# Optimization experiments

Measured on AMD Instinct MI355X. Metric: run time of the kernel, lower is better.

## Reference

```python
import jax, jax.numpy as jnp
import numpy as np

N_NEG = 60
TEMP = 0.07

def _normalize(x, axis):
    n = jnp.sqrt(jnp.sum(x * x, axis=axis, keepdims=True))
    return x / jnp.maximum(n, 1e-12)

def _grid_sample(img, grid):
    # img [B,C,H,W], grid [B,h,w,2] in [-1,1]; bilinear, padding_mode='border', align_corners=False
    B, C, H, W = img.shape
    ix = jnp.clip((grid[..., 0] + 1.0) * (W * 0.5) - 0.5, 0.0, W - 1.0)
    iy = jnp.clip((grid[..., 1] + 1.0) * (H * 0.5) - 0.5, 0.0, H - 1.0)
    x0 = jnp.floor(ix); y0 = jnp.floor(iy)
    x1 = jnp.minimum(x0 + 1.0, W - 1.0); y1 = jnp.minimum(y0 + 1.0, H - 1.0)
    wx = (ix - x0)[:, None]; wy = (iy - y0)[:, None]  # [B,1,h,w]
    imgf = img.reshape(B, C, H * W)
    hh, ww = grid.shape[1], grid.shape[2]
    def gat(yy, xx):
        idx = (yy * W + xx).astype(jnp.int32).reshape(B, 1, hh * ww)
        return jnp.take_along_axis(imgf, idx, axis=2).reshape(B, C, hh, ww)
    v00 = gat(y0, x0); v01 = gat(y0, x1); v10 = gat(y1, x0); v11 = gat(y1, x1)
    return (v00 * (1 - wx) * (1 - wy) + v01 * wx * (1 - wy)
            + v10 * (1 - wx) * wy + v11 * wx * wy)

def _forward(ref_fms, tgt_fms, target_l, target_r, queue):
    b, c, h, w = ref_fms.shape
    s = target_l.shape[-1] // w  # integer downscale factor (nearest interpolate == strided slice)
    disps_l = target_l[:, :, ::s, ::s] / float(s)   # [b,1,h,w]
    disps_r = target_r[:, :, ::s, ::s] / float(s)
    xb = jnp.broadcast_to(jnp.linspace(0.0, 1.0, w), (b, h, w))
    yb = jnp.broadcast_to(jnp.linspace(0.0, 1.0, h)[:, None], (b, h, w))

    def warp(img, disp):
        g = jnp.stack([xb + disp[:, 0] / w, yb], axis=-1)
        return _grid_sample(img, 2.0 * g - 1.0)

    # occlusion / validity mask (detached in the original)
    index = jnp.broadcast_to(jnp.arange(w, dtype=ref_fms.dtype), (b, 1, h, w))
    l2r2l = warp(warp(index, disps_r), -disps_l)
    masko = jnp.abs(index - l2r2l)[:, 0] < 3.0
    mask = masko & (disps_l[:, 0] > 0.0) & (xb - disps_l[:, 0] / w >= 0.0)
    mask = jax.lax.stop_gradient(mask).astype(ref_fms.dtype)  # [b,h,w]

    query = _normalize(ref_fms, 1)
    # positive: warp right feature to left view via disparity
    gpos = jnp.stack([xb - disps_l[:, 0] / w, yb], axis=-1)
    positive = _normalize(_grid_sample(tgt_fms, 2.0 * gpos - 1.0), 1)
    l_pos = jnp.einsum('bchw,bchw->bhw', query, positive)[..., None]

    # negatives: random integer pixel shifts around positive location
    # (no n_neg-fold repeat of tgt_fms; vmap grid_sample over the n axis instead)
    k1, k2 = jax.random.split(jax.random.key(1234))
    mag = jax.random.randint(k1, (b, h, w, N_NEG), 1, 25).astype(ref_fms.dtype)
    sgn = jnp.sign(jax.random.uniform(k2, (b, h, w, N_NEG)) - 0.5).astype(ref_fms.dtype)
    x_right = (xb - disps_l[:, 0] / w) * w
    fx = jnp.mod(x_right[..., None] + mag * sgn, float(w)) / w
    fy = fx / h  # faithful to original code (y coord reuses the normalized x coord)
    grids = jnp.moveaxis(jnp.stack([fx, fy], axis=-1), 3, 0)  # [n,b,h,w,2]
    neg = jax.vmap(lambda g: _grid_sample(tgt_fms, 2.0 * g - 1.0))(grids)  # [n,b,c,h,w]
    neg = _normalize(jnp.moveaxis(neg, 0, -1), 1)  # [b,c,h,w,n]
    l_neg = jnp.einsum('bchw,bchwn->bhwn', query, neg)

    qn = _normalize(queue, 0)  # forward re-normalizes the queue each call
    l_q = jnp.einsum('bchw,ck->bhwk', query, jax.lax.stop_gradient(qn))

    logits = jnp.concatenate([l_pos, l_neg, l_q], axis=-1) * mask[..., None]
    logits = logits.reshape(b * h * w, -1) / TEMP
    # CrossEntropyLoss with all-zero labels (positive is class 0)
    return jnp.mean(-jax.nn.log_softmax(logits, axis=-1)[:, 0])

def setup_inputs():
    key = jax.random.key(0)
    k1, k2, k3, k4, k5 = jax.random.split(key, 5)
    b, c, h, w = 2, 128, 64, 128
    H, W = 4 * h, 4 * w
    return {
        'ref_fms': jax.random.normal(k1, (b, c, h, w), jnp.float32),
        'tgt_fms': jax.random.normal(k2, (b, c, h, w), jnp.float32),
        'target_l': jax.random.uniform(k3, (b, 1, H, W), jnp.float32) * 64.0,
        'target_r': jax.random.uniform(k4, (b, 1, H, W), jnp.float32) * 64.0,
        'queue': jax.random.normal(k5, (c, 6000), jnp.float32),
    }

def reference(ref_fms, tgt_fms, target_l, target_r, queue):
    return _forward(ref_fms, tgt_fms, target_l, target_r, queue)
```

## Files before the change

### kernel.cpp

```cpp
#include <hip/hip_runtime.h>
#include <stdint.h>
#include <math.h>

#define HFM 64
#define WFM 128
#define CFM 128
#define BN 2
#define HWFM (HFM*WFM)
#define NPIX (BN*HWFM)
#define KQ 6000
#define KQP 6144
#define NNEG 60
#define NE (NPIX*NNEG)
#define EHALF_U 491520u
#define MSHIFT 15.0f
#define LOG2E 1.4426950408889634f

typedef _Float16 f16_8 __attribute__((ext_vector_type(8)));
typedef _Float16 f16_2 __attribute__((ext_vector_type(2)));
typedef float f32_4 __attribute__((ext_vector_type(4)));

__host__ __device__ __forceinline__ void threefry2x32(uint32_t k0, uint32_t k1,
                                                      uint32_t x0, uint32_t x1,
                                                      uint32_t* o0, uint32_t* o1) {
  uint32_t ks2 = k0 ^ k1 ^ 0x1BD11BDAu;
  x0 += k0; x1 += k1;
#define TFR(r) { x0 += x1; x1 = (x1 << (r)) | (x1 >> (32 - (r))); x1 ^= x0; }
  TFR(13) TFR(15) TFR(26) TFR(6)
  x0 += k1;  x1 += ks2 + 1u;
  TFR(17) TFR(29) TFR(16) TFR(24)
  x0 += ks2; x1 += k0 + 2u;
  TFR(13) TFR(15) TFR(26) TFR(6)
  x0 += k0;  x1 += k1 + 3u;
  TFR(17) TFR(29) TFR(16) TFR(24)
  x0 += k1;  x1 += ks2 + 4u;
  TFR(13) TFR(15) TFR(26) TFR(6)
  x0 += ks2; x1 += k0 + 5u;
#undef TFR
  *o0 = x0; *o1 = x1;
}

__device__ __forceinline__ void gs_coord(float t, float halfdim, float maxc,
                                         int* i0, int* i1, float* w) {
  float g = 2.0f * t - 1.0f;
  float x = (g + 1.0f) * halfdim - 0.5f;
  x = fminf(fmaxf(x, 0.0f), maxc);
  float f = floorf(x);
  *i0 = (int)f;
  *w = x - f;
  *i1 = (int)fminf(f + 1.0f, maxc);
}

__global__ __launch_bounds__(256) void k_A(
    const float* __restrict__ ref, const float* __restrict__ tgt,
    const float* __restrict__ queue,
    const float* __restrict__ target_l, const float* __restrict__ target_r,
    _Float16* __restrict__ refTf, _Float16* __restrict__ tgtTf,
    _Float16* __restrict__ queueTf, float2* __restrict__ qeb,
    float* __restrict__ maskArr, float* __restrict__ xr) {
  __shared__ float tile[64][35];
  int blk = blockIdx.x;
  int tid = threadIdx.x;
  if (blk < 64) {
    int p = blk * 256 + tid;
    int b = p >> 13;
    int rem = p & (HWFM - 1);
    int i = rem >> 7, j = rem & 127;
    const float stepx = 1.0f / 127.0f, stepy = 1.0f / 63.0f;
    float xb = (j == 127) ? 1.0f : j * stepx;
    float yb = (i == 63) ? 1.0f : i * stepy;
    const float* tl = target_l + (size_t)b * 256 * 512;
    const float* tr = target_r + (size_t)b * 256 * 512;
    float dl = tl[(4 * i) * 512 + 4 * j] * 0.25f;
    int y0i, y1i; float wy;
    gs_coord(yb, 32.0f, 63.0f, &y0i, &y1i, &wy);
    float t = xb - dl * (1.0f / 128.0f);
    int x0i, x1i; float wx;
    gs_coord(t, 64.0f, 127.0f, &x0i, &x1i, &wx);
    auto innerv = [&](int y, int x) -> float {
      float xbx = (x == 127) ? 1.0f : x * stepx;
      float drv = tr[(4 * y) * 512 + 4 * x] * 0.25f;
      float ti = xbx + drv * (1.0f / 128.0f);
      float g = 2.0f * ti - 1.0f;
      float ix2 = fminf(fmaxf((g + 1.0f) * 64.0f - 0.5f, 0.0f), 127.0f);
      float x0f = floorf(ix2);
      float wxp = ix2 - x0f;
      float x1f = fminf(x0f + 1.0f, 127.0f);
      return x0f * (1.0f - wxp) + x1f * wxp;
    };
    float v00 = innerv(y0i, x0i), v01 = innerv(y0i, x1i);
    float v10 = innerv(y1i, x0i), v11 = innerv(y1i, x1i);
    float l2r2l = v00 * (1.0f - wx) * (1.0f - wy) + v01 * wx * (1.0f - wy)
                + v10 * (1.0f - wx) * wy + v11 * wx * wy;
    bool masko = fabsf((float)j - l2r2l) < 3.0f;
    bool mk = masko && (dl > 0.0f) && (t >= 0.0f);
    maskArr[p] = mk ? 1.0f : 0.0f;
    xr[p] = t * 128.0f;
  } else if (blk < 88) {
    int k = (blk - 64) * 256 + tid;
    if (k < KQP) {
      if (k >= KQ) { qeb[k] = make_float2(0.0f, -1000.0f); }
      else {
        float ss = 0.0f;
        for (int c = 0; c < CFM; c++) { float v = queue[c * KQ + k]; ss += v * v; }
        float qi = 1.0f / fmaxf(sqrtf(ss), 1e-12f);
        qeb[k] = make_float2(qi * (LOG2E / 0.07f), -MSHIFT * LOG2E);
      }
    }
  } else if (blk < 472) {
    int q = blk - 88;
    int cy = q / 192, nx = q - cy * 192;
    int n0 = nx * 32, c0 = cy * 64;
    int c = tid >> 2, qq = tid & 3;
    const float* sp = queue + (size_t)(c0 + c) * KQ + n0 + qq * 4;
    if (n0 + 32 <= KQ) {
      float4 v0 = *(const float4*)sp;
      float4 v1 = *(const float4*)(sp + 16);
      tile[c][qq * 4 + 0] = v0.x; tile[c][qq * 4 + 1] = v0.y;
      tile[c][qq * 4 + 2] = v0.z; tile[c][qq * 4 + 3] = v0.w;
      tile[c][qq * 4 + 16] = v1.x; tile[c][qq * 4 + 17] = v1.y;
      tile[c][qq * 4 + 18] = v1.z; tile[c][qq * 4 + 19] = v1.w;
    } else {
#pragma unroll
      for (int k = 0; k < 4; k++) {
        int n = n0 + qq * 4 + k;
        tile[c][qq * 4 + k] = (n < KQ) ? sp[k] : 0.0f;
        tile[c][qq * 4 + 16 + k] = (n + 16 < KQ) ? sp[16 + k] : 0.0f;
      }
    }
    __syncthreads();
    int x = tid >> 3, j8 = tid & 7;
    f16_8 o;
#pragma unroll
    for (int k = 0; k < 8; k++) o[k] = (_Float16)tile[j8 * 8 + k][x];
    *(f16_8*)(queueTf + (size_t)(n0 + x) * CFM + c0 + j8 * 8) = o;
  } else {
    int fblk = blk - 472;
    int z = fblk >> 9, rem2 = fblk & 511;
    int cy = rem2 >> 8, xt = rem2 & 255;
    int x0 = xt * 32, c0 = cy * 64;
    int arr = z >> 1, b = z & 1;
    const float* src = (arr == 0 ? ref : tgt) + (size_t)b * CFM * HWFM;
    _Float16* dst = (arr == 0 ? refTf : tgtTf) + (size_t)b * HWFM * CFM;
    int c = tid >> 2, qq = tid & 3;
    const float* sp = src + (size_t)(c0 + c) * HWFM + x0 + qq * 4;
    float4 v0 = *(const float4*)sp;
    float4 v1 = *(const float4*)(sp + 16);
    tile[c][qq * 4 + 0] = v0.x; tile[c][qq * 4 + 1] = v0.y;
    tile[c][qq * 4 + 2] = v0.z; tile[c][qq * 4 + 3] = v0.w;
    tile[c][qq * 4 + 16] = v1.x; tile[c][qq * 4 + 17] = v1.y;
    tile[c][qq * 4 + 18] = v1.z; tile[c][qq * 4 + 19] = v1.w;
    __syncthreads();
    int x = tid >> 3, j8 = tid & 7;
    f16_8 o;
#pragma unroll
    for (int k = 0; k < 8; k++) o[k] = (_Float16)tile[j8 * 8 + k][x];
    *(f16_8*)(dst + (size_t)(x0 + x) * CFM + c0 + j8 * 8) = o;
  }
}

__global__ __launch_bounds__(256) void k_B(
    const _Float16* __restrict__ refTf, const _Float16* __restrict__ tgtTf,
    _Float16* __restrict__ QTf, float* __restrict__ stats,
    const float* __restrict__ maskArr, const float* __restrict__ xr,
    float* __restrict__ S, float* __restrict__ logit0,
    int* __restrict__ count, int* __restrict__ list) {
  __shared__ int wsum[4];
  int blk = blockIdx.x;
  int tid = threadIdx.x;
  int lane = tid & 63;
  if (blk == 0) {
    int wave = tid >> 6;
    int base_p = tid * 64;
    unsigned long long bits = 0ull;
    const float4* m4 = (const float4*)(maskArr + base_p);
#pragma unroll
    for (int k = 0; k < 16; k++) {
      float4 v = m4[k];
      if (v.x > 0.0f) bits |= 1ull << (4 * k + 0);
      if (v.y > 0.0f) bits |= 1ull << (4 * k + 1);
      if (v.z > 0.0f) bits |= 1ull << (4 * k + 2);
      if (v.w > 0.0f) bits |= 1ull << (4 * k + 3);
    }
    int m = __popcll(bits);
    int scan = m;
#pragma unroll
    for (int off = 1; off < 64; off <<= 1) {
      int n = __shfl_up(scan, off, 64);
      if (lane >= off) scan += n;
    }
    if (lane == 63) wsum[wave] = scan;
    __syncthreads();
    int wbase = 0;
    for (int w = 0; w < wave; w++) wbase += wsum[w];
    int idx = wbase + scan - m;
    for (int k = 0; k < 64; k++) {
      if ((bits >> k) & 1ull) list[idx++] = base_p + k;
    }
    if (tid == 255) *count = idx;
  } else if (blk < 65) {
    int sub = tid >> 6;
    int xg = (blk - 1) * 4 + sub;
    int b = xg >> 7, x = xg & 127;
    int xp = min(x + 1, 127);
    int c2 = lane * 2;
    int base = b * HWFM;
    f16_2 c0  = *(const f16_2*)(tgtTf + (size_t)(base + x) * CFM + c2);
    f16_2 c1  = *(const f16_2*)(tgtTf + (size_t)(base + WFM + x) * CFM + c2);
    f16_2 c0p = *(const f16_2*)(tgtTf + (size_t)(base + xp) * CFM + c2);
    f16_2 c1p = *(const f16_2*)(tgtTf + (size_t)(base + WFM + xp) * CFM + c2);
    float a0 = (float)c0[0], a1 = (float)c0[1];
    float b0 = (float)c1[0], b1 = (float)c1[1];
    float p0 = (float)c0p[0], p1 = (float)c0p[1];
    float q0 = (float)c1p[0], q1 = (float)c1p[1];
    float s[7];
    s[0] = a0 * a0 + a1 * a1;
    s[1] = a0 * b0 + a1 * b1;
    s[2] = b0 * b0 + b1 * b1;
    s[3] = a0 * p0 + a1 * p1;
    s[4] = a0 * q0 + a1 * q1;
    s[5] = b0 * p0 + b1 * p1;
    s[6] = b0 * q0 + b1 * q1;
#pragma unroll
    for (int o = 32; o; o >>= 1)
#pragma unroll
      for (int k = 0; k < 7; k++) s[k] += __shfl_xor(s[k], o, 64);
    if (lane == 0) {
      float* st = stats + (size_t)xg * 8;
#pragma unroll
      for (int k = 0; k < 7; k++) st[k] = s[k];
      st[7] = 0.0f;
    }
  } else {
    int wave = tid >> 6;
    int p = (blk - 65) * 4 + wave;
    float mk = maskArr[p];
    if (mk == 0.0f) return;
    int b = p >> 13;
    int rem = p & (HWFM - 1);
    int i = rem >> 7;
    const float stepy = 1.0f / 63.0f;
    float yb = (i == 63) ? 1.0f : i * stepy;
    float t = xr[p] * (1.0f / 128.0f);
    int y0i, y1i; float wy;
    gs_coord(yb, 32.0f, 63.0f, &y0i, &y1i, &wy);
    int x0i, x1i; float wx;
    gs_coord(t, 64.0f, 127.0f, &x0i, &x1i, &wx);

    int c2 = lane * 2;
    f16_2 q2 = *(const f16_2*)(refTf + (size_t)p * CFM + c2);
    int bo = b * HWFM;
    f16_2 a2 = *(const f16_2*)(tgtTf + (size_t)(bo + y0i * WFM + x0i) * CFM + c2);
    f16_2 b2 = *(const f16_2*)(tgtTf + (size_t)(bo + y0i * WFM + x1i) * CFM + c2);
    f16_2 cc2 = *(const f16_2*)(tgtTf + (size_t)(bo + y1i * WFM + x0i) * CFM + c2);
    f16_2 d2 = *(const f16_2*)(tgtTf + (size_t)(bo + y1i * WFM + x1i) * CFM + c2);

    float w00 = (1.0f - wx) * (1.0f - wy), w01 = wx * (1.0f - wy);
    float w10 = (1.0f - wx) * wy,          w11 = wx * wy;
    float q0 = (float)q2[0], q1 = (float)q2[1];
    float v0 = w00 * (float)a2[0] + w01 * (float)b2[0] + w10 * (float)cc2[0] + w11 * (float)d2[0];
    float v1 = w00 * (float)a2[1] + w01 * (float)b2[1] + w10 * (float)cc2[1] + w11 * (float)d2[1];

    float s0 = q0 * q0 + q1 * q1;
    float s1 = q0 * v0 + q1 * v1;
    float s2 = v0 * v0 + v1 * v1;
#pragma unroll
    for (int o = 32; o; o >>= 1) {
      s0 += __shfl_xor(s0, o, 64);
      s1 += __shfl_xor(s1, o, 64);
      s2 += __shfl_xor(s2, o, 64);
    }
    float inv = 1.0f / fmaxf(sqrtf(s0), 1e-12f);
    f16_2 qw; qw[0] = (_Float16)(q0 * inv); qw[1] = (_Float16)(q1 * inv);
    *(f16_2*)(QTf + (size_t)p * CFM + c2) = qw;
    if (lane == 0) {
      float lpos = (s1 * inv) / fmaxf(sqrtf(s2), 1e-12f);
      float lg0 = lpos / 0.07f;
      logit0[p] = lg0;
      S[p] = expf(lg0 - MSHIFT);
    }
  }
}

__global__ __launch_bounds__(256, 4) void k_gemm(
    const _Float16* __restrict__ QTf,
    const _Float16* __restrict__ queueTf,
    const _Float16* __restrict__ tgtTf,
    const float2* __restrict__ qeb,
    float* __restrict__ S, float* __restrict__ D,
    const int* __restrict__ count, const int* __restrict__ list) {
  __shared__ _Float16 Bs[2][64 * CFM];
  __shared__ float Srow[64];
  int tid = threadIdx.x;
  int cnt = *count;
  int split = blockIdx.x;
  int slot0 = blockIdx.y * 64;
  if (slot0 >= cnt) return;
  bool isD = (split == 12);
  int wave = tid >> 6, lane = tid & 63;
  int quad = lane >> 4, l16 = lane & 15;
  int wm = wave >> 1, wn = wave & 1;

  if (tid < 64) Srow[tid] = 0.0f;

  int lrow = lane >> 4, lchunk = lane & 15;
  auto stage = [&](const _Float16* bsrc, int buf) {
#pragma unroll
    for (int i = 0; i < 4; i++) {
      int rb = wave * 16 + i * 4;
      int r = rb + lrow;
      const _Float16* g = bsrc + (size_t)r * CFM + ((lchunk ^ (r & 7)) << 3);
      __builtin_amdgcn_global_load_lds(
          (const __attribute__((address_space(1))) void*)g,
          (__attribute__((address_space(3))) void*)(&Bs[buf][rb * CFM]),
          16, 0, 0);
    }
  };
  auto bpanel = [&](int ic) -> const _Float16* {
    if (!isD) return queueTf + (size_t)(split * 512 + ic * 64) * CFM;
    return tgtTf + ((size_t)(ic >> 2) * HWFM + (ic & 3) * 64) * CFM;
  };

  stage(bpanel(0), 0);

  f16_8 Af[2][4];
  int r0 = slot0 + wm * 32;
#pragma unroll
  for (int mt = 0; mt < 2; mt++) {
    int prow = list[min(r0 + mt * 16 + l16, cnt - 1)];
    const _Float16* arow = QTf + (size_t)prow * CFM + quad * 8;
#pragma unroll
    for (int ks = 0; ks < 4; ks++)
      Af[mt][ks] = *(const f16_8*)(arow + ks * 32);
  }
  int pbv[2][4];
  if (isD) {
#pragma unroll
    for (int mt = 0; mt < 2; mt++)
#pragma unroll
      for (int r = 0; r < 4; r++)
        pbv[mt][r] = list[min(r0 + mt * 16 + quad * 4 + r, cnt - 1)] >> 13;
  }

  __syncthreads();
  int cur = 0;
  float rowsum[2][4] = {{0.0f,0.0f,0.0f,0.0f},{0.0f,0.0f,0.0f,0.0f}};

#pragma unroll
  for (int ic = 0; ic < 8; ic++) {
    if (ic + 1 < 8) stage(bpanel(ic + 1), cur ^ 1);
    float2 qb[2];
    if (!isD) {
      int n0 = split * 512 + ic * 64 + wn * 32;
#pragma unroll
      for (int nt = 0; nt < 2; nt++) qb[nt] = qeb[n0 + nt * 16 + l16];
    }
    f32_4 acc[2][2];
#pragma unroll
    for (int mt = 0; mt < 2; mt++)
#pragma unroll
      for (int nt = 0; nt < 2; nt++)
        acc[mt][nt] = (f32_4){0.0f, 0.0f, 0.0f, 0.0f};
#pragma unroll
    for (int ks = 0; ks < 4; ks++) {
      f16_8 Bk[2];
#pragma unroll
      for (int nt = 0; nt < 2; nt++) {
        int brow = wn * 32 + nt * 16 + l16;
        Bk[nt] = *(const f16_8*)(&Bs[cur][brow * CFM + ((ks * 32 + quad * 8) ^ ((brow & 7) * 8))]);
      }
#pragma unroll
      for (int mt = 0; mt < 2; mt++)
#pragma unroll
        for (int nt = 0; nt < 2; nt++)
          acc[mt][nt] = __builtin_amdgcn_mfma_f32_16x16x32_f16(Af[mt][ks], Bk[nt], acc[mt][nt], 0, 0, 0);
    }
    if (!isD) {
#pragma unroll
      for (int nt = 0; nt < 2; nt++)
#pragma unroll
        for (int mt = 0; mt < 2; mt++)
#pragma unroll
          for (int r = 0; r < 4; r++)
            rowsum[mt][r] += exp2f(fmaf(acc[mt][nt][r], qb[nt].x, qb[nt].y));
    } else {
      int batch = ic >> 2;
#pragma unroll
      for (int mt = 0; mt < 2; mt++)
#pragma unroll
        for (int nt = 0; nt < 2; nt++)
#pragma unroll
          for (int r = 0; r < 4; r++) {
            int sl = slot0 + wm * 32 + mt * 16 + quad * 4 + r;
            int colL = (ic & 3) * 64 + wn * 32 + nt * 16 + l16;
            if (sl < cnt && pbv[mt][r] == batch)
              D[(size_t)sl * 256 + colL] = acc[mt][nt][r];
          }
    }
    __syncthreads();
    cur ^= 1;
  }

  if (!isD) {
#pragma unroll
    for (int mt = 0; mt < 2; mt++)
#pragma unroll
      for (int r = 0; r < 4; r++) {
        float vv = rowsum[mt][r];
        vv += __shfl_xor(vv, 1);
        vv += __shfl_xor(vv, 2);
        vv += __shfl_xor(vv, 4);
        vv += __shfl_xor(vv, 8);
        rowsum[mt][r] = vv;
      }
    if (l16 == 0) {
#pragma unroll
      for (int mt = 0; mt < 2; mt++)
#pragma unroll
        for (int r = 0; r < 4; r++)
          atomicAdd(&Srow[wm * 32 + mt * 16 + quad * 4 + r], rowsum[mt][r]);
    }
    __syncthreads();
    if (tid < 64) {
      int pr = slot0 + tid;
      if (pr < cnt) atomicAdd(&S[list[pr]], Srow[tid]);
    }
  }
}

__global__ __launch_bounds__(256) void k_negatives_lite(
    const float* __restrict__ D, const float* __restrict__ stats,
    const float* __restrict__ xr, float* __restrict__ S,
    const int* __restrict__ count, const int* __restrict__ list,
    uint32_t k1a, uint32_t k1b, uint32_t k2a, uint32_t k2b) {
  int tid = threadIdx.x;
  int wave = tid >> 6, lane = tid & 63;
  int cnt = *count;
  int slot = blockIdx.x * 4 + wave;
  if (slot >= cnt) return;
  int p = list[slot];
  int b = p >> 13;
  float esum = 0.0f;
  if (lane < NNEG) {
    uint32_t e = (uint32_t)(p * NNEG + lane);
    uint32_t h0, h1;
    threefry2x32(k1a, k1b, e, e + (uint32_t)NE, &h0, &h1);
    uint32_t off = ((h0 % 24u) * 16u + (h1 % 24u)) % 24u;
    float mag = (float)(1u + off);
    uint32_t ub;
    {
      uint32_t a, bm;
      if (e < EHALF_U) { threefry2x32(k2a, k2b, e, e + EHALF_U, &a, &bm); ub = a; }
      else             { threefry2x32(k2a, k2b, e - EHALF_U, e, &a, &bm); ub = bm; }
    }
    float u = __uint_as_float((ub >> 9) | 0x3F800000u) - 1.0f;
    float sg = (u > 0.5f) ? 1.0f : ((u < 0.5f) ? -1.0f : 0.0f);

    float v = xr[p] + mag * sg;
    float r = fmodf(v, 128.0f);
    if (r < 0.0f) r += 128.0f;
    float fx = r * (1.0f / 128.0f);
    float fy = fx * (1.0f / 64.0f);
    int x0i, x1i, y0i, y1i; float wx, wy;
    gs_coord(fx, 64.0f, 127.0f, &x0i, &x1i, &wx);
    gs_coord(fy, 32.0f, 63.0f, &y0i, &y1i, &wy);

    const float* Dp = D + (size_t)slot * 256;
    float d00 = Dp[x0i], d01 = Dp[x1i];
    float d10 = Dp[128 + x0i], d11 = Dp[128 + x1i];
    float u0 = 1.0f - wy, u1 = wy;
    float dv0 = u0 * d00 + u1 * d10;
    float dv1 = u0 * d01 + u1 * d11;
    float dot = (1.0f - wx) * dv0 + wx * dv1;

    const float* st0 = stats + (size_t)(b * 128 + x0i) * 8;
    const float* st1 = stats + (size_t)(b * 128 + x1i) * 8;
    float4 sa = *(const float4*)st0;
    float4 sb = *(const float4*)(st0 + 4);
    float4 sc = *(const float4*)st1;
    float a0 = u0 * u0, a1 = u0 * u1, a2 = u1 * u1;
    float nB0 = a0 * sa.x + 2.0f * a1 * sa.y + a2 * sa.z;
    float nB1 = a0 * sc.x + 2.0f * a1 * sc.y + a2 * sc.z;
    float cB  = a0 * sa.w + a1 * (sb.x + sb.y) + a2 * sb.z;
    float wx0 = 1.0f - wx;
    float nsq = wx0 * wx0 * nB0 + 2.0f * wx * wx0 * cB + wx * wx * nB1;
    float ln = dot / fmaxf(sqrtf(fmaxf(nsq, 0.0f)), 1e-12f);
    esum = __expf(ln * (1.0f / 0.07f) - MSHIFT);
  }
#pragma unroll
  for (int o = 32; o; o >>= 1) esum += __shfl_xor(esum, o, 64);
  if (lane == 0) atomicAdd(&S[p], esum);
}

__global__ __launch_bounds__(1024) void k_finalize(
    const float* __restrict__ S, const float* __restrict__ logit0,
    const float* __restrict__ maskArr, float* __restrict__ out) {
  int tid = threadIdx.x;
  const float cmask = logf(6061.0f);
  double acc = 0.0;
  for (int p = tid; p < NPIX; p += 1024) {
    float term = (maskArr[p] > 0.0f) ? (logf(S[p]) + MSHIFT - logit0[p]) : cmask;
    acc += (double)term;
  }
#pragma unroll
  for (int off = 32; off; off >>= 1) acc += __shfl_down(acc, off, 64);
  __shared__ double sd[16];
  if ((tid & 63) == 0) sd[tid >> 6] = acc;
  __syncthreads();
  if (tid == 0) {
    double tot = 0.0;
    for (int w = 0; w < 16; w++) tot += sd[w];
    out[0] = (float)(tot / (double)NPIX);
  }
}

extern "C" void kernel_launch(void* const* d_in, const int* in_sizes, int n_in,
                              void* d_out, int out_size, void* d_ws, size_t ws_size,
                              hipStream_t stream) {
  const float* ref   = (const float*)d_in[0];
  const float* tgt   = (const float*)d_in[1];
  const float* tl    = (const float*)d_in[2];
  const float* tr    = (const float*)d_in[3];
  const float* queue = (const float*)d_in[4];
  float* out = (float*)d_out;
  float* ws = (float*)d_ws;

  float2* qeb = (float2*)ws;
  float* S    = ws + 12288;
  float* lg0  = ws + 28672;
  float* mk   = ws + 45056;
  float* xr   = ws + 61440;
  int* count  = (int*)(ws + 77824);
  int* list   = (int*)(ws + 77840);
  _Float16* QTf     = (_Float16*)(ws + 94464);
  _Float16* queueTf = (_Float16*)(ws + 1143040);
  _Float16* tgtTf   = (_Float16*)(ws + 1536256);
  _Float16* refTf   = (_Float16*)(ws + 2584832);
  float* stats = ws + 3633408;
  float* D     = ws + 3635456;

  uint32_t b0o0, b0o1, b1o0, b1o1;
  threefry2x32(0u, 1234u, 0u, 2u, &b0o0, &b0o1);
  threefry2x32(0u, 1234u, 1u, 3u, &b1o0, &b1o1);
  uint32_t k1a = b0o0, k1b = b1o0, k2a = b0o1, k2b = b1o1;

  k_A<<<dim3(2520), dim3(256), 0, stream>>>(ref, tgt, queue, tl, tr,
                                            refTf, tgtTf, queueTf, qeb, mk, xr);
  k_B<<<dim3(65 + 4096), dim3(256), 0, stream>>>(refTf, tgtTf, QTf, stats,
                                                 mk, xr, S, lg0, count, list);
  k_gemm<<<dim3(13, 256), dim3(256), 0, stream>>>(QTf, queueTf, tgtTf, qeb,
                                                  S, D, count, list);
  k_negatives_lite<<<dim3(NPIX / 4), dim3(256), 0, stream>>>(D, stats, xr, S, count, list,
                                                             k1a, k1b, k2a, k2b);
  k_finalize<<<dim3(1), dim3(1024), 0, stream>>>(S, lg0, mk, out);
}
```

Before: 127.3 us.

## Rebalance GEMM work split and parallelize final loss reduction across blocks

```diff
diff --git a/kernel.cpp b/kernel.cpp
--- a/kernel.cpp
+++ b/kernel.cpp
@@ -57,7 +57,8 @@
     const float* __restrict__ target_l, const float* __restrict__ target_r,
     _Float16* __restrict__ refTf, _Float16* __restrict__ tgtTf,
     _Float16* __restrict__ queueTf, float2* __restrict__ qeb,
-    float* __restrict__ maskArr, float* __restrict__ xr) {
+    float* __restrict__ maskArr, float* __restrict__ xr,
+    double* __restrict__ dacc, int* __restrict__ dctr) {
   __shared__ float tile[64][35];
   int blk = blockIdx.x;
   int tid = threadIdx.x;
@@ -97,6 +98,7 @@
     maskArr[p] = mk ? 1.0f : 0.0f;
     xr[p] = t * 128.0f;
   } else if (blk < 88) {
+    if (blk == 64 && tid == 0) { *dacc = 0.0; *dctr = 0; }
     int k = (blk - 64) * 256 + tid;
     if (k < KQP) {
       if (k >= KQ) { qeb[k] = make_float2(0.0f, -1000.0f); }
@@ -293,13 +295,14 @@
   __shared__ float Srow[64];
   int tid = threadIdx.x;
   int cnt = *count;
-  int split = blockIdx.x;
-  int slot0 = blockIdx.y * 64;
+  int split = blockIdx.x & 7;
+  int slot0 = (blockIdx.x >> 3) * 64;
   if (slot0 >= cnt) return;
-  bool isD = (split == 12);
   int wave = tid >> 6, lane = tid & 63;
   int quad = lane >> 4, l16 = lane & 15;
   int wm = wave >> 1, wn = wave & 1;
+  int dbatch = split >> 2;
+  int dxoff = (split & 3) * 64;
 
   if (tid < 64) Srow[tid] = 0.0f;
 
@@ -317,8 +320,8 @@
     }
   };
   auto bpanel = [&](int ic) -> const _Float16* {
-    if (!isD) return queueTf + (size_t)(split * 512 + ic * 64) * CFM;
-    return tgtTf + ((size_t)(ic >> 2) * HWFM + (ic & 3) * 64) * CFM;
+    if (ic < 12) return queueTf + (size_t)(split * 768 + ic * 64) * CFM;
+    return tgtTf + ((size_t)dbatch * HWFM + dxoff) * CFM;
   };
 
   stage(bpanel(0), 0);
@@ -334,24 +337,21 @@
       Af[mt][ks] = *(const f16_8*)(arow + ks * 32);
   }
   int pbv[2][4];
-  if (isD) {
-#pragma unroll
-    for (int mt = 0; mt < 2; mt++)
-#pragma unroll
-      for (int r = 0; r < 4; r++)
-        pbv[mt][r] = list[min(r0 + mt * 16 + quad * 4 + r, cnt - 1)] >> 13;
-  }
+#pragma unroll
+  for (int mt = 0; mt < 2; mt++)
+#pragma unroll
+    for (int r = 0; r < 4; r++)
+      pbv[mt][r] = list[min(r0 + mt * 16 + quad * 4 + r, cnt - 1)] >> 13;
 
   __syncthreads();
   int cur = 0;
   float rowsum[2][4] = {{0.0f,0.0f,0.0f,0.0f},{0.0f,0.0f,0.0f,0.0f}};
 
-#pragma unroll
-  for (int ic = 0; ic < 8; ic++) {
-    if (ic + 1 < 8) stage(bpanel(ic + 1), cur ^ 1);
+  for (int ic = 0; ic < 13; ic++) {
+    if (ic + 1 < 13) stage(bpanel(ic + 1), cur ^ 1);
     float2 qb[2];
-    if (!isD) {
-      int n0 = split * 512 + ic * 64 + wn * 32;
+    if (ic < 12) {
+      int n0 = split * 768 + ic * 64 + wn * 32;
 #pragma unroll
       for (int nt = 0; nt < 2; nt++) qb[nt] = qeb[n0 + nt * 16 + l16];
     }
@@ -375,7 +375,7 @@
         for (int nt = 0; nt < 2; nt++)
           acc[mt][nt] = __builtin_amdgcn_mfma_f32_16x16x32_f16(Af[mt][ks], Bk[nt], acc[mt][nt], 0, 0, 0);
     }
-    if (!isD) {
+    if (ic < 12) {
 #pragma unroll
       for (int nt = 0; nt < 2; nt++)
 #pragma unroll
@@ -384,7 +384,6 @@
           for (int r = 0; r < 4; r++)
             rowsum[mt][r] += exp2f(fmaf(acc[mt][nt][r], qb[nt].x, qb[nt].y));
     } else {
-      int batch = ic >> 2;
 #pragma unroll
       for (int mt = 0; mt < 2; mt++)
 #pragma unroll
@@ -392,8 +391,8 @@
 #pragma unroll
           for (int r = 0; r < 4; r++) {
             int sl = slot0 + wm * 32 + mt * 16 + quad * 4 + r;
-            int colL = (ic & 3) * 64 + wn * 32 + nt * 16 + l16;
-            if (sl < cnt && pbv[mt][r] == batch)
+            int colL = dxoff + wn * 32 + nt * 16 + l16;
+            if (sl < cnt && pbv[mt][r] == dbatch)
               D[(size_t)sl * 256 + colL] = acc[mt][nt][r];
           }
     }
@@ -401,30 +400,28 @@
     cur ^= 1;
   }
 
-  if (!isD) {
+#pragma unroll
+  for (int mt = 0; mt < 2; mt++)
+#pragma unroll
+    for (int r = 0; r < 4; r++) {
+      float vv = rowsum[mt][r];
+      vv += __shfl_xor(vv, 1);
+      vv += __shfl_xor(vv, 2);
+      vv += __shfl_xor(vv, 4);
+      vv += __shfl_xor(vv, 8);
+      rowsum[mt][r] = vv;
+    }
+  if (l16 == 0) {
 #pragma unroll
     for (int mt = 0; mt < 2; mt++)
 #pragma unroll
-      for (int r = 0; r < 4; r++) {
-        float vv = rowsum[mt][r];
-        vv += __shfl_xor(vv, 1);
-        vv += __shfl_xor(vv, 2);
-        vv += __shfl_xor(vv, 4);
-        vv += __shfl_xor(vv, 8);
-        rowsum[mt][r] = vv;
-      }
-    if (l16 == 0) {
-#pragma unroll
-      for (int mt = 0; mt < 2; mt++)
-#pragma unroll
-        for (int r = 0; r < 4; r++)
-          atomicAdd(&Srow[wm * 32 + mt * 16 + quad * 4 + r], rowsum[mt][r]);
-    }
-    __syncthreads();
-    if (tid < 64) {
-      int pr = slot0 + tid;
-      if (pr < cnt) atomicAdd(&S[list[pr]], Srow[tid]);
-    }
+      for (int r = 0; r < 4; r++)
+        atomicAdd(&Srow[wm * 32 + mt * 16 + quad * 4 + r], rowsum[mt][r]);
+  }
+  __syncthreads();
+  if (tid < 64) {
+    int pr = slot0 + tid;
+    if (pr < cnt) atomicAdd(&S[list[pr]], Srow[tid]);
   }
 }
 
@@ -494,14 +491,13 @@
 
 __global__ __launch_bounds__(1024) void k_finalize(
     const float* __restrict__ S, const float* __restrict__ logit0,
-    const float* __restrict__ maskArr, float* __restrict__ out) {
+    const float* __restrict__ maskArr, float* __restrict__ out,
+    double* __restrict__ dacc, int* __restrict__ dctr) {
   int tid = threadIdx.x;
   const float cmask = logf(6061.0f);
-  double acc = 0.0;
-  for (int p = tid; p < NPIX; p += 1024) {
-    float term = (maskArr[p] > 0.0f) ? (logf(S[p]) + MSHIFT - logit0[p]) : cmask;
-    acc += (double)term;
-  }
+  int p = blockIdx.x * 1024 + tid;
+  float term = (maskArr[p] > 0.0f) ? (logf(S[p]) + MSHIFT - logit0[p]) : cmask;
+  double acc = (double)term;
 #pragma unroll
   for (int off = 32; off; off >>= 1) acc += __shfl_down(acc, off, 64);
   __shared__ double sd[16];
@@ -510,7 +506,13 @@
   if (tid == 0) {
     double tot = 0.0;
     for (int w = 0; w < 16; w++) tot += sd[w];
-    out[0] = (float)(tot / (double)NPIX);
+    atomicAdd(dacc, tot);
+    __threadfence();
+    int old = atomicAdd(dctr, 1);
+    if (old == 15) {
+      __threadfence();
+      out[0] = (float)(*(volatile double*)dacc / (double)NPIX);
+    }
   }
 }
 
@@ -531,6 +533,8 @@
   float* mk   = ws + 45056;
   float* xr   = ws + 61440;
   int* count  = (int*)(ws + 77824);
+  double* dacc = (double*)(ws + 77826);
+  int* dctr   = (int*)(ws + 77828);
   int* list   = (int*)(ws + 77840);
   _Float16* QTf     = (_Float16*)(ws + 94464);
   _Float16* queueTf = (_Float16*)(ws + 1143040);
@@ -545,12 +549,13 @@
   uint32_t k1a = b0o0, k1b = b1o0, k2a = b0o1, k2b = b1o1;
 
   k_A<<<dim3(2520), dim3(256), 0, stream>>>(ref, tgt, queue, tl, tr,
-                                            refTf, tgtTf, queueTf, qeb, mk, xr);
+                                            refTf, tgtTf, queueTf, qeb, mk, xr,
+                                            dacc, dctr);
   k_B<<<dim3(65 + 4096), dim3(256), 0, stream>>>(refTf, tgtTf, QTf, stats,
                                                  mk, xr, S, lg0, count, list);
-  k_gemm<<<dim3(13, 256), dim3(256), 0, stream>>>(QTf, queueTf, tgtTf, qeb,
-                                                  S, D, count, list);
+  k_gemm<<<dim3(2048), dim3(256), 0, stream>>>(QTf, queueTf, tgtTf, qeb,
+                                               S, D, count, list);
   k_negatives_lite<<<dim3(NPIX / 4), dim3(256), 0, stream>>>(D, stats, xr, S, count, list,
                                                              k1a, k1b, k2a, k2b);
-  k_finalize<<<dim3(1), dim3(1024), 0, stream>>>(S, lg0, mk, out);
-}
+  k_finalize<<<dim3(16), dim3(1024), 0, stream>>>(S, lg0, mk, out, dacc, dctr);
+}
```

Result: faster. 115.9 us (-8.9%).
